# Optimization experiments

Hardware: AMD Instinct MI355X
Metric: run time of the kernel (lower is better)

Reference implementation:

```python
import jax, jax.numpy as jnp
import numpy as np

VOCAB = 40000
EMB = 128
INNER = 128
Q_LEN = 20


def setup_inputs() -> dict:
    key = jax.random.key(0)
    ks = jax.random.split(key, 16)
    B, S, NB = 32, 512, 20
    std = 0.1
    inp = {
        "memories": jax.random.normal(ks[0], (B, S, NB, EMB), jnp.float32),
        "stories": jax.random.normal(ks[1], (B, S, EMB), jnp.float32),
        "stories_mask": jnp.ones((B, S), jnp.float32),
        "queries": jax.random.randint(ks[2], (B, Q_LEN), 0, VOCAB, jnp.int32),
        "keys": jax.random.randint(ks[3], (NB,), 0, VOCAB, jnp.int32),
        # learned parameters
        "emb_table": jax.random.normal(ks[4], (VOCAB, EMB), jnp.float32) * std,
        "mult_mask": jnp.ones((Q_LEN, EMB), jnp.float32),
        "A": jax.random.normal(ks[5], (EMB, INNER), jnp.float32) * std,
        "Bm": jax.random.normal(ks[6], (EMB, INNER), jnp.float32) * std,
        "C": jax.random.normal(ks[7], (EMB, INNER), jnp.float32) * std,
        "v": jnp.ones((INNER,), jnp.float32),
        "D": jax.random.normal(ks[8], (EMB, INNER), jnp.float32) * std,
        "E": jax.random.normal(ks[9], (EMB, INNER), jnp.float32) * std,
        "F": jax.random.normal(ks[10], (EMB, INNER), jnp.float32) * std,
        "w": jnp.ones((INNER,), jnp.float32),
        "H": jax.random.normal(ks[11], (EMB, EMB), jnp.float32) * std,
        "R": jax.random.normal(ks[12], (EMB, VOCAB), jnp.float32) * std,
    }
    return inp


def reference(memories, stories, stories_mask, queries, keys,
              emb_table, mult_mask, A, Bm, C, v, D, E, F, w, H, R):
    # _reduce_query: embed tokens, apply positional multiplicative mask, sum over positions
    u = jnp.sum(emb_table[queries] * mult_mask, axis=1)            # [B, emb]

    # intratemporal (Bahdanau-style) attention over memory blocks
    ia = jnp.einsum('bsne,ei->bsni', memories, A)                  # [B,S,NB,inner]
    kb = emb_table[keys] @ Bm                                      # [NB,inner]
    qc = u @ C                                                     # [B,inner]
    intr_align = jnp.sum(v * jnp.tanh(ia + kb[None, None] + qc[:, None, None]), axis=3)  # [B,S,NB]
    intr_attn = jax.nn.softmax(intr_align, axis=2)[..., None]      # [B,S,NB,1]
    temporal_memory = jnp.sum(intr_attn * memories, axis=2)        # [B,S,emb]

    # temporal attention over story sentences (with sentence term E, softmax activation)
    td = temporal_memory @ D                                       # [B,S,inner]
    te = stories @ E                                               # [B,S,inner]
    tf = (u @ F)[:, None]                                          # [B,1,inner]
    temporal_align_unmasked = jnp.sum(w * jnp.tanh(td + te + tf), axis=2)  # [B,S]
    temporal_align = temporal_align_unmasked * stories_mask
    # softmax branch: additive -inf mask where stories_mask == 0 (inf*0 NaNs zeroed in torch)
    masked_logits = jnp.where(stories_mask != 0, temporal_align, -jnp.inf)
    temporal_attn = jax.nn.softmax(masked_logits, axis=1)          # [B,S]

    # output readout (standard memory-network head)
    o = jnp.sum(temporal_attn[..., None] * temporal_memory, axis=1)  # [B,emb]
    logits = (o + u @ H) @ R                                         # [B,vocab]
    return logits
```

## Files before the change

### kernel.cpp

```cpp
#include <hip/hip_runtime.h>
#include <hip/hip_bf16.h>

#define B_   32
#define S_   512
#define NB_  20
#define EMB_ 128
#define VOC_ 40000

typedef float f32x4 __attribute__((ext_vector_type(4)));
typedef _Float16 f16x8 __attribute__((ext_vector_type(8)));
typedef __fp16 fp16x2 __attribute__((ext_vector_type(2)));

union FragH { uint4 u; f16x8 h; };
union H2 { fp16x2 h; unsigned u; };

__device__ __forceinline__ unsigned pk2(float a, float b){
  H2 t; t.h = __builtin_amdgcn_cvt_pkrtz(a, b);
  return t.u;
}
__device__ __forceinline__ unsigned short f2h(float x){
  _Float16 h = (_Float16)x;
  return __builtin_bit_cast(unsigned short, h);
}
__device__ __forceinline__ float tanh_fast(float x){
  float xx = fminf(fmaxf(x, -15.f), 15.f);
  float e2 = __builtin_amdgcn_exp2f(xx * 2.8853900817779268f);
  float r  = __builtin_amdgcn_rcpf(e2 + 1.f);
  return fmaf(-2.f, r, 1.f);
}


__global__ __launch_bounds__(128) void prep_kernel(
    const int* __restrict__ queries, const int* __restrict__ keys,
    const float* __restrict__ emb, const float* __restrict__ mmask,
    const float* __restrict__ A, const float* __restrict__ Bm,
    const float* __restrict__ C, const float* __restrict__ D,
    const float* __restrict__ E, const float* __restrict__ F,
    const float* __restrict__ H,
    float* __restrict__ qc_w, float* __restrict__ tf_w,
    float* __restrict__ uh_w, float* __restrict__ kb_w,
    unsigned short* __restrict__ afrag, unsigned short* __restrict__ w2frag)
{
  int bid = blockIdx.x, tid = threadIdx.x;
  if (bid < 32) {
    __shared__ float ulds[128];
    int b = bid;
    float s = 0.f;
    for (int q=0;q<NB_;q++){
      int tok = queries[b*NB_+q];
      s += emb[tok*128+tid]*mmask[q*128+tid];
    }
    ulds[tid] = s;
    __syncthreads();
    float sq=0.f, sf=0.f, sh=0.f;
    for (int e=0;e<128;e++){
      float uv = ulds[e];
      sq += uv*C[e*128+tid];
      sf += uv*F[e*128+tid];
      sh += uv*H[e*128+tid];
    }
    qc_w[b*128+tid]=sq; tf_w[b*128+tid]=sf; uh_w[b*128+tid]=sh;
  } else if (bid < 52) {
    __shared__ float ek[128];
    int n = bid-32;
    int tok = keys[n];
    ek[tid] = emb[tok*128+tid];
    __syncthreads();
    float s=0.f;
    for (int e=0;e<128;e++) s += ek[e]*Bm[e*128+tid];
    kb_w[n*128+tid] = s;
  } else if (bid < 60) {
    int a = bid-52;
    for (int cc=0;cc<2;cc++){
      int c = (a*128+tid)*2+cc;
      int lane = c&63, kc = (c>>6)&3, nt = c>>8;
      int n2 = nt*16 + (lane&15);
      int k0 = kc*32 + (lane>>4)*8;
      alignas(16) unsigned short t[8];
      #pragma unroll
      for (int j=0;j<8;j++) t[j] = f2h(A[(k0+j)*128+n2]);
      *(uint4*)(afrag + c*8) = *(const uint4*)t;
    }
  } else {
    int wb = bid-60;
    for (int cc=0;cc<2;cc++){
      int c = (wb*128+tid)*2+cc;
      int lane = c&63, kc = (c>>6)&7, nt = c>>9;
      int n2 = nt*16 + (lane&15);
      int k0 = kc*32 + (lane>>4)*8;
      alignas(16) unsigned short t[8];
      #pragma unroll
      for (int j=0;j<8;j++){
        int k = k0+j;
        float x = (k<128) ? D[k*128+n2] : E[(k-128)*128+n2];
        t[j] = f2h(x);
      }
      *(uint4*)(w2frag + c*8) = *(const uint4*)t;
    }
  }
}

__global__ __launch_bounds__(256) void k2_kernel(
    const float* __restrict__ mem, const unsigned short* __restrict__ afrag,
    const float* __restrict__ kb_w, const float* __restrict__ qc_w,
    const float* __restrict__ vvec,
    const float* __restrict__ stories, const unsigned short* __restrict__ w2frag,
    const float* __restrict__ tf_w, const float* __restrict__ wvec,
    const float* __restrict__ smask,
    unsigned short* __restrict__ tm_h, float* __restrict__ talign_w)
{
  __shared__ unsigned short mfr[5*4*64*8];
  __shared__ float alignP[4*80];
  __shared__ float aligns[80];
  __shared__ float attns[80];
  __shared__ float partial2[16];

  int g = blockIdx.x, tid = threadIdx.x;
  int b = g >> 7;

  int p2 = tid>>6, e0 = (tid&63)*2;
  float2 sto = *(const float2*)(stories + ((size_t)(g*4+p2))*128 + e0);

  {
    int kq = (tid&31)*4;
    int kgs = kq>>5, s2s = (kq>>3)&3, offs = kq&7;
    int r0 = tid>>5;
    int cbs = s2s ^ ((kgs&1)<<2);
    int slot_e = (s2s<<4) | ((r0 ^ cbs) & 15);
    int slot_o = (s2s<<4) | (((r0^8) ^ cbs) & 15);
    unsigned addr_e = (unsigned)((kgs*64 + slot_e)*16 + offs*2);
    unsigned addr_o = (unsigned)((kgs*64 + slot_o)*16 + offs*2);
    const float4* gm = (const float4*)(mem) + (size_t)g*2560 + tid;
    #pragma unroll
    for (int mt=0; mt<5; ++mt){
      float4 d0 = gm[(2*mt)*256];
      float4 d1 = gm[(2*mt+1)*256];
      *(uint2*)((char*)mfr + addr_e + mt*4096) = make_uint2(pk2(d0.x,d0.y), pk2(d0.z,d0.w));
      *(uint2*)((char*)mfr + addr_o + mt*4096) = make_uint2(pk2(d1.x,d1.y), pk2(d1.z,d1.w));
    }
  }
  __syncthreads();

  int w = tid>>6, lane = tid&63;
  int lo16 = lane & 15, hi16 = lane >> 4;

  {
    f32x4 acc[5][2];
    #pragma unroll
    for (int mt=0;mt<5;mt++){ acc[mt][0]=(f32x4)(0.f); acc[mt][1]=(f32x4)(0.f); }

    #pragma unroll
    for (int kc=0;kc<4;kc++){
      FragH b0, b1;
      b0.u = *(const uint4*)(afrag + ((size_t)((2*w)*4+kc)*64 + lane)*8);
      b1.u = *(const uint4*)(afrag + ((size_t)((2*w+1)*4+kc)*64 + lane)*8);
      int slot = (hi16<<4) | ((lo16 ^ hi16 ^ ((kc&1)<<2)) & 15);
      #pragma unroll
      for (int mt=0;mt<5;mt++){
        FragH a;
        a.u = *(const uint4*)(mfr + ((mt*4+kc)*64 + slot)*8);
        acc[mt][0] = __builtin_amdgcn_mfma_f32_16x16x32_f16(a.h, b0.h, acc[mt][0], 0,0,0);
        acc[mt][1] = __builtin_amdgcn_mfma_f32_16x16x32_f16(a.h, b1.h, acc[mt][1], 0,0,0);
      }
    }

    int i0 = w*32 + lo16, i1 = i0 + 16;
    float qc0 = qc_w[b*128+i0], qc1 = qc_w[b*128+i1];
    float vv0 = vvec[i0],       vv1 = vvec[i1];
    const float* kb0 = kb_w + i0;
    #pragma unroll
    for (int mt=0;mt<5;mt++){
      #pragma unroll
      for (int r=0;r<4;r++){
        unsigned row = mt*16 + hi16*4 + r;
        unsigned p = row/20u;
        unsigned n = row - p*20u;
        float z0 = acc[mt][0][r] + kb0[n*128]    + qc0;
        float z1 = acc[mt][1][r] + kb0[n*128+16] + qc1;
        float part = vv0*tanh_fast(z0) + vv1*tanh_fast(z1);
        part += __shfl_xor(part, 1);
        part += __shfl_xor(part, 2);
        part += __shfl_xor(part, 4);
        part += __shfl_xor(part, 8);
        if (lo16 == 0) alignP[w*80+row] = part;
      }
    }
  }
  __syncthreads();
  if (tid < 80){
    aligns[tid] = alignP[tid] + alignP[80+tid] + alignP[160+tid] + alignP[240+tid];
  }
  __syncthreads();
  if (tid < 4){
    float mx = -1e30f;
    for (int n=0;n<NB_;n++) mx = fmaxf(mx, aligns[tid*NB_+n]);
    float s = 0.f;
    for (int n=0;n<NB_;n++){ float e = __expf(aligns[tid*NB_+n]-mx); attns[tid*NB_+n]=e; s+=e; }
    float inv = 1.f/s;
    for (int n=0;n<NB_;n++) attns[tid*NB_+n] *= inv;
  }
  __syncthreads();

  unsigned otm;
  {
    int kg = e0>>5, s2 = (e0>>3)&3;
    int cb = s2 ^ ((kg&1)<<2);
    unsigned base = (unsigned)((kg*64 + (s2<<4))*16 + (e0&7)*2);
    float2 o = make_float2(0.f,0.f);
    #define TM_STEP(ROW) { \
      H2 q; q.u = *(const unsigned*)((const char*)mfr + base + (((ROW)>>4)*4096) + ((((ROW)&15) ^ cb) & 15)*16); \
      float a = attns[(ROW)]; \
      o.x += a*(float)q.h[0]; \
      o.y += a*(float)q.h[1]; }
    #define TM_20(P) { \
      TM_STEP((P)*20+0)  TM_STEP((P)*20+1)  TM_STEP((P)*20+2)  TM_STEP((P)*20+3)  \
      TM_STEP((P)*20+4)  TM_STEP((P)*20+5)  TM_STEP((P)*20+6)  TM_STEP((P)*20+7)  \
      TM_STEP((P)*20+8)  TM_STEP((P)*20+9)  TM_STEP((P)*20+10) TM_STEP((P)*20+11) \
      TM_STEP((P)*20+12) TM_STEP((P)*20+13) TM_STEP((P)*20+14) TM_STEP((P)*20+15) \
      TM_STEP((P)*20+16) TM_STEP((P)*20+17) TM_STEP((P)*20+18) TM_STEP((P)*20+19) }
    switch(p2){
      case 0: TM_20(0) break;
      case 1: TM_20(1) break;
      case 2: TM_20(2) break;
      default: TM_20(3) break;
    }
    otm = pk2(o.x, o.y);
    *(unsigned*)(tm_h + ((size_t)g*4+p2)*128 + e0) = otm;
  }
  __syncthreads();

  {
    int kc = e0>>5;
    int lane2 = (((e0>>3)&3)<<4) | p2;
    *(unsigned*)(mfr + (kc*64+lane2)*8 + (e0&7)) = otm;
    *(unsigned*)(mfr + ((kc+4)*64+lane2)*8 + (e0&7)) = pk2(sto.x, sto.y);
  }
  __syncthreads();

  {
    f32x4 acc0 = (f32x4)(0.f), acc1 = (f32x4)(0.f);
    #pragma unroll
    for (int kc=0;kc<8;kc++){
      FragH af, b0, b1;
      af.u = *(const uint4*)(mfr + (kc*64+lane)*8);
      b0.u = *(const uint4*)(w2frag + ((size_t)((2*w)*8+kc)*64+lane)*8);
      b1.u = *(const uint4*)(w2frag + ((size_t)((2*w+1)*8+kc)*64+lane)*8);
      acc0 = __builtin_amdgcn_mfma_f32_16x16x32_f16(af.h, b0.h, acc0, 0,0,0);
      acc1 = __builtin_amdgcn_mfma_f32_16x16x32_f16(af.h, b1.h, acc1, 0,0,0);
    }
    if (hi16 == 0){
      #pragma unroll
      for (int r=0;r<4;r++){
        int i0 = (2*w)*16+lo16;
        float part = wvec[i0]*tanh_fast(acc0[r] + tf_w[b*128+i0]);
        int i1 = (2*w+1)*16+lo16;
        part += wvec[i1]*tanh_fast(acc1[r] + tf_w[b*128+i1]);
        part += __shfl_xor(part,1);
        part += __shfl_xor(part,2);
        part += __shfl_xor(part,4);
        part += __shfl_xor(part,8);
        if (lo16==0) partial2[w*4+r] = part;
      }
    }
  }
  __syncthreads();
  if (tid<4){
    float ta = partial2[tid]+partial2[4+tid]+partial2[8+tid]+partial2[12+tid];
    int flat = g*4+tid;
    float m = smask[flat];
    talign_w[flat] = (m != 0.0f) ? ta*m : -INFINITY;
  }
}

__global__ __launch_bounds__(256) void k3_kernel(
    const float* __restrict__ talign_w, const unsigned short* __restrict__ tm_h,
    const float* __restrict__ uh_w, float* __restrict__ ov_w)
{
  __shared__ float attn[512];
  __shared__ float red[256];
  __shared__ float2 red2[256];
  int bid = blockIdx.x, tid = threadIdx.x;
  int b = bid >> 3, ec = bid & 7;

  float v0 = talign_w[b*512+tid];
  float v1 = talign_w[b*512+256+tid];
  red[tid] = fmaxf(v0,v1);
  __syncthreads();
  for (int s=128;s>0;s>>=1){ if (tid<s) red[tid]=fmaxf(red[tid],red[tid+s]); __syncthreads(); }
  float M = red[0];
  __syncthreads();
  float e0v = __expf(v0-M), e1v = __expf(v1-M);
  red[tid] = e0v+e1v;
  __syncthreads();
  for (int s=128;s>0;s>>=1){ if (tid<s) red[tid]+=red[tid+s]; __syncthreads(); }
  float invZ = 1.f/red[0];
  attn[tid] = e0v*invZ;
  attn[256+tid] = e1v*invZ;
  __syncthreads();

  int e = ec*16 + (tid&7)*2;
  int sg = tid>>3;
  const unsigned short* tmb = tm_h + ((size_t)b*512 + sg*16)*128 + e;
  float2 a2 = make_float2(0.f,0.f);
  #pragma unroll 8
  for (int i=0;i<16;i++){
    H2 q; q.u = *(const unsigned*)(tmb + (size_t)i*128);
    float at = attn[sg*16+i];
    a2.x += at*(float)q.h[0];
    a2.y += at*(float)q.h[1];
  }
  red2[tid] = a2;
  __syncthreads();
  for (int s=128;s>=8;s>>=1){
    if (tid<s){ red2[tid].x += red2[tid+s].x; red2[tid].y += red2[tid+s].y; }
    __syncthreads();
  }
  if (tid<8){
    int e2 = ec*16 + tid*2;
    ov_w[b*128+e2]   = red2[tid].x + uh_w[b*128+e2];
    ov_w[b*128+e2+1] = red2[tid].y + uh_w[b*128+e2+1];
  }
}

__global__ __launch_bounds__(256) void k4_kernel(
    const float* __restrict__ ov_w, const float* __restrict__ R,
    float* __restrict__ out)
{
  int tid = threadIdx.x;
  int j = blockIdx.x*128 + (tid&63)*2;
  if (j >= VOC_) return;
  int bh = tid>>6;
  const float* ovb = ov_w + bh*8*128;
  float2 acc[8];
  #pragma unroll
  for (int bb=0;bb<8;bb++) acc[bb]=make_float2(0.f,0.f);
  for (int e=0;e<128;e+=4){
    float2 r0 = *(const float2*)(&R[(size_t)(e+0)*VOC_ + j]);
    float2 r1 = *(const float2*)(&R[(size_t)(e+1)*VOC_ + j]);
    float2 r2 = *(const float2*)(&R[(size_t)(e+2)*VOC_ + j]);
    float2 r3 = *(const float2*)(&R[(size_t)(e+3)*VOC_ + j]);
    #pragma unroll
    for (int bb=0;bb<8;bb++){
      float4 o = *(const float4*)(&ovb[bb*128+e]);
      acc[bb].x += o.x*r0.x + o.y*r1.x + o.z*r2.x + o.w*r3.x;
      acc[bb].y += o.x*r0.y + o.y*r1.y + o.z*r2.y + o.w*r3.y;
    }
  }
  #pragma unroll
  for (int bb=0;bb<8;bb++)
    *(float2*)(&out[(size_t)(bh*8+bb)*VOC_ + j]) = acc[bb];
}

extern "C" void kernel_launch(void* const* d_in, const int* in_sizes, int n_in,
                              void* d_out, int out_size, void* d_ws, size_t ws_size,
                              hipStream_t stream)
{
  const float* mem    = (const float*)d_in[0];
  const float* stories= (const float*)d_in[1];
  const float* smask  = (const float*)d_in[2];
  const int*   queries= (const int*)d_in[3];
  const int*   keys   = (const int*)d_in[4];
  const float* emb    = (const float*)d_in[5];
  const float* mmask  = (const float*)d_in[6];
  const float* A      = (const float*)d_in[7];
  const float* Bm     = (const float*)d_in[8];
  const float* C      = (const float*)d_in[9];
  const float* vvec   = (const float*)d_in[10];
  const float* D      = (const float*)d_in[11];
  const float* E      = (const float*)d_in[12];
  const float* F      = (const float*)d_in[13];
  const float* wvec   = (const float*)d_in[14];
  const float* H      = (const float*)d_in[15];
  const float* R      = (const float*)d_in[16];
  float* out = (float*)d_out;

  char* ws = (char*)d_ws;
  float* qc_w             = (float*)(ws + 0);
  float* tf_w             = (float*)(ws + 16384);
  float* uh_w             = (float*)(ws + 32768);
  float* kb_w             = (float*)(ws + 49152);
  unsigned short* afrag   = (unsigned short*)(ws + 60416);
  unsigned short* w2frag  = (unsigned short*)(ws + 93184);
  unsigned short* tm_h    = (unsigned short*)(ws + 158720);
  float* talign_w         = (float*)(ws + 4353024);
  float* ov_w             = (float*)(ws + 4418560);

  prep_kernel<<<76,128,0,stream>>>(queries, keys, emb, mmask, A, Bm, C, D, E, F, H,
                                   qc_w, tf_w, uh_w, kb_w, afrag, w2frag);
  k2_kernel<<<4096,256,0,stream>>>(mem, afrag, kb_w, qc_w, vvec,
                                   stories, w2frag, tf_w, wvec, smask,
                                   tm_h, talign_w);
  k3_kernel<<<256,256,0,stream>>>(talign_w, tm_h, uh_w, ov_w);
  k4_kernel<<<313,256,0,stream>>>(ov_w, R, out);
}
```

Measured before the change: 368.5 us.

## Process four tiles per block in k2 with register prefetch of next memory tile

k2 now loops over four consecutive 4-sentence tiles per block, with a quarter as many blocks. While the current tile is being computed, the next tile's memories and stories are loaded into registers and written to LDS once the current tile has finished reading it. The A-weight fragments and per-batch vectors are loaded into registers once per block instead of once per tile. The softmax is now a wave-parallel shuffle reduction rather than four serial threads, and a separate LDS buffer holds the second GEMM's operands. The aim is to hide global-memory latency and amortise setup, at the cost of higher register pressure (launch_bounds 256,4) and fewer blocks to balance across CUs.

```diff
diff --git a/kernel.cpp b/kernel.cpp
--- a/kernel.cpp
+++ b/kernel.cpp
@@ -100,7 +100,7 @@
   }
 }
 
-__global__ __launch_bounds__(256) void k2_kernel(
+__global__ __launch_bounds__(256,4) void k2_kernel(
     const float* __restrict__ mem, const unsigned short* __restrict__ afrag,
     const float* __restrict__ kb_w, const float* __restrict__ qc_w,
     const float* __restrict__ vvec,
@@ -110,64 +110,90 @@
     unsigned short* __restrict__ tm_h, float* __restrict__ talign_w)
 {
   __shared__ unsigned short mfr[5*4*64*8];
+  __shared__ unsigned short a2f[512*8];
   __shared__ float alignP[4*80];
-  __shared__ float aligns[80];
   __shared__ float attns[80];
   __shared__ float partial2[16];
 
-  int g = blockIdx.x, tid = threadIdx.x;
-  int b = g >> 7;
-
-  int p2 = tid>>6, e0 = (tid&63)*2;
-  float2 sto = *(const float2*)(stories + ((size_t)(g*4+p2))*128 + e0);
-
-  {
-    int kq = (tid&31)*4;
-    int kgs = kq>>5, s2s = (kq>>3)&3, offs = kq&7;
-    int r0 = tid>>5;
-    int cbs = s2s ^ ((kgs&1)<<2);
-    int slot_e = (s2s<<4) | ((r0 ^ cbs) & 15);
-    int slot_o = (s2s<<4) | (((r0^8) ^ cbs) & 15);
-    unsigned addr_e = (unsigned)((kgs*64 + slot_e)*16 + offs*2);
-    unsigned addr_o = (unsigned)((kgs*64 + slot_o)*16 + offs*2);
-    const float4* gm = (const float4*)(mem) + (size_t)g*2560 + tid;
-    #pragma unroll
-    for (int mt=0; mt<5; ++mt){
-      float4 d0 = gm[(2*mt)*256];
-      float4 d1 = gm[(2*mt+1)*256];
-      *(uint2*)((char*)mfr + addr_e + mt*4096) = make_uint2(pk2(d0.x,d0.y), pk2(d0.z,d0.w));
-      *(uint2*)((char*)mfr + addr_o + mt*4096) = make_uint2(pk2(d1.x,d1.y), pk2(d1.z,d1.w));
-    }
-  }
-  __syncthreads();
+  const int T = 4;
+  int tid = threadIdx.x;
+  int g0 = blockIdx.x * T;
+  int b = g0 >> 7;
 
   int w = tid>>6, lane = tid&63;
   int lo16 = lane & 15, hi16 = lane >> 4;
-
-  {
+  int p2 = tid>>6, e0 = (tid&63)*2;
+
+  int kq = (tid&31)*4;
+  int kgs = kq>>5, s2s = (kq>>3)&3, offs = kq&7;
+  int r0 = tid>>5;
+  int cbs = s2s ^ ((kgs&1)<<2);
+  unsigned addr_e = (unsigned)((kgs*64 + ((s2s<<4) | ((r0 ^ cbs) & 15)))*16 + offs*2);
+  unsigned addr_o = (unsigned)((kgs*64 + ((s2s<<4) | (((r0^8) ^ cbs) & 15)))*16 + offs*2);
+
+  int i0 = w*32 + lo16, i1 = i0 + 16;
+  float qc0 = qc_w[b*128+i0], qc1 = qc_w[b*128+i1];
+  float vv0 = vvec[i0],       vv1 = vvec[i1];
+  float tf0 = tf_w[b*128+i0], tf1 = tf_w[b*128+i1];
+  float wv0 = wvec[i0],       wv1 = wvec[i1];
+  const float* kb0 = kb_w + i0;
+
+  FragH bf0[4], bf1[4];
+  #pragma unroll
+  for (int kc=0;kc<4;kc++){
+    bf0[kc].u = *(const uint4*)(afrag + ((size_t)((2*w)*4+kc)*64 + lane)*8);
+    bf1[kc].u = *(const uint4*)(afrag + ((size_t)((2*w+1)*4+kc)*64 + lane)*8);
+  }
+
+  float4 pf[10];
+  float2 sto, sto_n;
+
+  auto load_tile = [&](int g){
+    const float4* gmt = (const float4*)(mem) + (size_t)g*2560 + tid;
+    #pragma unroll
+    for (int mt=0;mt<5;mt++){
+      pf[2*mt]   = gmt[(2*mt)*256];
+      pf[2*mt+1] = gmt[(2*mt+1)*256];
+    }
+  };
+  auto store_tile = [&](){
+    #pragma unroll
+    for (int mt=0;mt<5;mt++){
+      *(uint2*)((char*)mfr + addr_e + mt*4096) =
+          make_uint2(pk2(pf[2*mt].x,pf[2*mt].y), pk2(pf[2*mt].z,pf[2*mt].w));
+      *(uint2*)((char*)mfr + addr_o + mt*4096) =
+          make_uint2(pk2(pf[2*mt+1].x,pf[2*mt+1].y), pk2(pf[2*mt+1].z,pf[2*mt+1].w));
+    }
+  };
+
+  load_tile(g0);
+  sto = *(const float2*)(stories + ((size_t)(g0*4+p2))*128 + e0);
+  store_tile();
+  __syncthreads();
+
+  for (int t=0; t<T; ++t){
+    int g = g0 + t;
+
     f32x4 acc[5][2];
     #pragma unroll
     for (int mt=0;mt<5;mt++){ acc[mt][0]=(f32x4)(0.f); acc[mt][1]=(f32x4)(0.f); }
-
     #pragma unroll
     for (int kc=0;kc<4;kc++){
-      FragH b0, b1;
-      b0.u = *(const uint4*)(afrag + ((size_t)((2*w)*4+kc)*64 + lane)*8);
-      b1.u = *(const uint4*)(afrag + ((size_t)((2*w+1)*4+kc)*64 + lane)*8);
       int slot = (hi16<<4) | ((lo16 ^ hi16 ^ ((kc&1)<<2)) & 15);
       #pragma unroll
       for (int mt=0;mt<5;mt++){
         FragH a;
         a.u = *(const uint4*)(mfr + ((mt*4+kc)*64 + slot)*8);
-        acc[mt][0] = __builtin_amdgcn_mfma_f32_16x16x32_f16(a.h, b0.h, acc[mt][0], 0,0,0);
-        acc[mt][1] = __builtin_amdgcn_mfma_f32_16x16x32_f16(a.h, b1.h, acc[mt][1], 0,0,0);
-      }
-    }
-
-    int i0 = w*32 + lo16, i1 = i0 + 16;
-    float qc0 = qc_w[b*128+i0], qc1 = qc_w[b*128+i1];
-    float vv0 = vvec[i0],       vv1 = vvec[i1];
-    const float* kb0 = kb_w + i0;
+        acc[mt][0] = __builtin_amdgcn_mfma_f32_16x16x32_f16(a.h, bf0[kc].h, acc[mt][0], 0,0,0);
+        acc[mt][1] = __builtin_amdgcn_mfma_f32_16x16x32_f16(a.h, bf1[kc].h, acc[mt][1], 0,0,0);
+      }
+    }
+    if (t > 0 && tid < 4){
+      float ta = partial2[tid]+partial2[4+tid]+partial2[8+tid]+partial2[12+tid];
+      int flat = (g-1)*4+tid;
+      float m = smask[flat];
+      talign_w[flat] = (m != 0.0f) ? ta*m : -INFINITY;
+    }
     #pragma unroll
     for (int mt=0;mt<5;mt++){
       #pragma unroll
@@ -185,88 +211,94 @@
         if (lo16 == 0) alignP[w*80+row] = part;
       }
     }
-  }
-  __syncthreads();
-  if (tid < 80){
-    aligns[tid] = alignP[tid] + alignP[80+tid] + alignP[160+tid] + alignP[240+tid];
-  }
-  __syncthreads();
+    __syncthreads();
+
+    if (t+1 < T){
+      load_tile(g+1);
+      sto_n = *(const float2*)(stories + ((size_t)((g+1)*4+p2))*128 + e0);
+    }
+    {
+      float av = -1e30f;
+      if (lane < 20){
+        int idx = w*20 + lane;
+        av = alignP[idx] + alignP[80+idx] + alignP[160+idx] + alignP[240+idx];
+      }
+      float mx = av;
+      #pragma unroll
+      for (int d=1; d<32; d<<=1) mx = fmaxf(mx, __shfl_xor(mx, d));
+      mx = fmaxf(mx, __shfl_xor(mx, 32));
+      float ev = (lane<20) ? __expf(av - mx) : 0.f;
+      float sm = ev;
+      #pragma unroll
+      for (int d=1; d<64; d<<=1) sm += __shfl_xor(sm, d);
+      if (lane<20) attns[w*20+lane] = ev * __builtin_amdgcn_rcpf(sm);
+    }
+    __syncthreads();
+
+    unsigned otm;
+    {
+      int kg = e0>>5, s2 = (e0>>3)&3;
+      int cb = s2 ^ ((kg&1)<<2);
+      unsigned base = (unsigned)((kg*64 + (s2<<4))*16 + (e0&7)*2);
+      float2 o = make_float2(0.f,0.f);
+      #define TM_STEP(ROW) { \
+        H2 q; q.u = *(const unsigned*)((const char*)mfr + base + (((ROW)>>4)*4096) + ((((ROW)&15) ^ cb) & 15)*16); \
+        float a = attns[(ROW)]; \
+        o.x += a*(float)q.h[0]; \
+        o.y += a*(float)q.h[1]; }
+      #define TM_20(P) { \
+        TM_STEP((P)*20+0)  TM_STEP((P)*20+1)  TM_STEP((P)*20+2)  TM_STEP((P)*20+3)  \
+        TM_STEP((P)*20+4)  TM_STEP((P)*20+5)  TM_STEP((P)*20+6)  TM_STEP((P)*20+7)  \
+        TM_STEP((P)*20+8)  TM_STEP((P)*20+9)  TM_STEP((P)*20+10) TM_STEP((P)*20+11) \
+        TM_STEP((P)*20+12) TM_STEP((P)*20+13) TM_STEP((P)*20+14) TM_STEP((P)*20+15) \
+        TM_STEP((P)*20+16) TM_STEP((P)*20+17) TM_STEP((P)*20+18) TM_STEP((P)*20+19) }
+      switch(p2){
+        case 0: TM_20(0) break;
+        case 1: TM_20(1) break;
+        case 2: TM_20(2) break;
+        default: TM_20(3) break;
+      }
+      otm = pk2(o.x, o.y);
+      *(unsigned*)(tm_h + ((size_t)g*4+p2)*128 + e0) = otm;
+      int kcA = e0>>5;
+      int lane2 = (((e0>>3)&3)<<4) | p2;
+      *(unsigned*)(a2f + (kcA*64+lane2)*8 + (e0&7)) = otm;
+      *(unsigned*)(a2f + ((kcA+4)*64+lane2)*8 + (e0&7)) = pk2(sto.x, sto.y);
+    }
+    __syncthreads();
+
+    if (t+1 < T){
+      store_tile();
+      sto = sto_n;
+    }
+    {
+      f32x4 acc0 = (f32x4)(0.f), acc1 = (f32x4)(0.f);
+      #pragma unroll
+      for (int kc=0;kc<8;kc++){
+        FragH af, b0, b1;
+        af.u = *(const uint4*)(a2f + (kc*64+lane)*8);
+        b0.u = *(const uint4*)(w2frag + ((size_t)((2*w)*8+kc)*64+lane)*8);
+        b1.u = *(const uint4*)(w2frag + ((size_t)((2*w+1)*8+kc)*64+lane)*8);
+        acc0 = __builtin_amdgcn_mfma_f32_16x16x32_f16(af.h, b0.h, acc0, 0,0,0);
+        acc1 = __builtin_amdgcn_mfma_f32_16x16x32_f16(af.h, b1.h, acc1, 0,0,0);
+      }
+      if (hi16 == 0){
+        #pragma unroll
+        for (int r=0;r<4;r++){
+          float part = wv0*tanh_fast(acc0[r] + tf0) + wv1*tanh_fast(acc1[r] + tf1);
+          part += __shfl_xor(part,1);
+          part += __shfl_xor(part,2);
+          part += __shfl_xor(part,4);
+          part += __shfl_xor(part,8);
+          if (lo16==0) partial2[w*4+r] = part;
+        }
+      }
+    }
+    __syncthreads();
+  }
   if (tid < 4){
-    float mx = -1e30f;
-    for (int n=0;n<NB_;n++) mx = fmaxf(mx, aligns[tid*NB_+n]);
-    float s = 0.f;
-    for (int n=0;n<NB_;n++){ float e = __expf(aligns[tid*NB_+n]-mx); attns[tid*NB_+n]=e; s+=e; }
-    float inv = 1.f/s;
-    for (int n=0;n<NB_;n++) attns[tid*NB_+n] *= inv;
-  }
-  __syncthreads();
-
-  unsigned otm;
-  {
-    int kg = e0>>5, s2 = (e0>>3)&3;
-    int cb = s2 ^ ((kg&1)<<2);
-    unsigned base = (unsigned)((kg*64 + (s2<<4))*16 + (e0&7)*2);
-    float2 o = make_float2(0.f,0.f);
-    #define TM_STEP(ROW) { \
-      H2 q; q.u = *(const unsigned*)((const char*)mfr + base + (((ROW)>>4)*4096) + ((((ROW)&15) ^ cb) & 15)*16); \
-      float a = attns[(ROW)]; \
-      o.x += a*(float)q.h[0]; \
-      o.y += a*(float)q.h[1]; }
-    #define TM_20(P) { \
-      TM_STEP((P)*20+0)  TM_STEP((P)*20+1)  TM_STEP((P)*20+2)  TM_STEP((P)*20+3)  \
-      TM_STEP((P)*20+4)  TM_STEP((P)*20+5)  TM_STEP((P)*20+6)  TM_STEP((P)*20+7)  \
-      TM_STEP((P)*20+8)  TM_STEP((P)*20+9)  TM_STEP((P)*20+10) TM_STEP((P)*20+11) \
-      TM_STEP((P)*20+12) TM_STEP((P)*20+13) TM_STEP((P)*20+14) TM_STEP((P)*20+15) \
-      TM_STEP((P)*20+16) TM_STEP((P)*20+17) TM_STEP((P)*20+18) TM_STEP((P)*20+19) }
-    switch(p2){
-      case 0: TM_20(0) break;
-      case 1: TM_20(1) break;
-      case 2: TM_20(2) break;
-      default: TM_20(3) break;
-    }
-    otm = pk2(o.x, o.y);
-    *(unsigned*)(tm_h + ((size_t)g*4+p2)*128 + e0) = otm;
-  }
-  __syncthreads();
-
-  {
-    int kc = e0>>5;
-    int lane2 = (((e0>>3)&3)<<4) | p2;
-    *(unsigned*)(mfr + (kc*64+lane2)*8 + (e0&7)) = otm;
-    *(unsigned*)(mfr + ((kc+4)*64+lane2)*8 + (e0&7)) = pk2(sto.x, sto.y);
-  }
-  __syncthreads();
-
-  {
-    f32x4 acc0 = (f32x4)(0.f), acc1 = (f32x4)(0.f);
-    #pragma unroll
-    for (int kc=0;kc<8;kc++){
-      FragH af, b0, b1;
-      af.u = *(const uint4*)(mfr + (kc*64+lane)*8);
-      b0.u = *(const uint4*)(w2frag + ((size_t)((2*w)*8+kc)*64+lane)*8);
-      b1.u = *(const uint4*)(w2frag + ((size_t)((2*w+1)*8+kc)*64+lane)*8);
-      acc0 = __builtin_amdgcn_mfma_f32_16x16x32_f16(af.h, b0.h, acc0, 0,0,0);
-      acc1 = __builtin_amdgcn_mfma_f32_16x16x32_f16(af.h, b1.h, acc1, 0,0,0);
-    }
-    if (hi16 == 0){
-      #pragma unroll
-      for (int r=0;r<4;r++){
-        int i0 = (2*w)*16+lo16;
-        float part = wvec[i0]*tanh_fast(acc0[r] + tf_w[b*128+i0]);
-        int i1 = (2*w+1)*16+lo16;
-        part += wvec[i1]*tanh_fast(acc1[r] + tf_w[b*128+i1]);
-        part += __shfl_xor(part,1);
-        part += __shfl_xor(part,2);
-        part += __shfl_xor(part,4);
-        part += __shfl_xor(part,8);
-        if (lo16==0) partial2[w*4+r] = part;
-      }
-    }
-  }
-  __syncthreads();
-  if (tid<4){
     float ta = partial2[tid]+partial2[4+tid]+partial2[8+tid]+partial2[12+tid];
-    int flat = g*4+tid;
+    int flat = (g0+T-1)*4+tid;
     float m = smask[flat];
     talign_w[flat] = (m != 0.0f) ? ta*m : -INFINITY;
   }
@@ -387,7 +419,7 @@
 
   prep_kernel<<<76,128,0,stream>>>(queries, keys, emb, mmask, A, Bm, C, D, E, F, H,
                                    qc_w, tf_w, uh_w, kb_w, afrag, w2frag);
-  k2_kernel<<<4096,256,0,stream>>>(mem, afrag, kb_w, qc_w, vvec,
+  k2_kernel<<<1024,256,0,stream>>>(mem, afrag, kb_w, qc_w, vvec,
                                    stories, w2frag, tf_w, wvec, smask,
                                    tm_h, talign_w);
   k3_kernel<<<256,256,0,stream>>>(talign_w, tm_h, uh_w, ov_w);
```

Measured after the change: 503.4 us. 36.6% more time.

## Precombine key and query bias per batch, warp-level softmax, trim tanh clamp

Applied to the files above, without the earlier changes.

The prep kernel now builds a combined per-batch, per-block bias table (kb + qc) across 640 extra blocks, so the main kernel adds one value instead of two and drops the division that mapped a row to its block index. The three-step block softmax (shared-memory reduction plus four serial threads) becomes a per-wave shuffle reduction, which removes a __syncthreads barrier. Loop-invariant vector loads are hoisted, and the clamp inside tanh_fast is removed; without it, large arguments rely on exp2 overflowing to infinity and the reciprocal then giving zero. The cost is a larger prep launch and a bigger bias table to read in the main kernel.

```diff
diff --git a/kernel.cpp b/kernel.cpp
--- a/kernel.cpp
+++ b/kernel.cpp
@@ -23,8 +23,7 @@
   return __builtin_bit_cast(unsigned short, h);
 }
 __device__ __forceinline__ float tanh_fast(float x){
-  float xx = fminf(fmaxf(x, -15.f), 15.f);
-  float e2 = __builtin_amdgcn_exp2f(xx * 2.8853900817779268f);
+  float e2 = __builtin_amdgcn_exp2f(x * 2.8853900817779268f);
   float r  = __builtin_amdgcn_rcpf(e2 + 1.f);
   return fmaf(-2.f, r, 1.f);
 }
@@ -37,8 +36,8 @@
     const float* __restrict__ C, const float* __restrict__ D,
     const float* __restrict__ E, const float* __restrict__ F,
     const float* __restrict__ H,
-    float* __restrict__ qc_w, float* __restrict__ tf_w,
-    float* __restrict__ uh_w, float* __restrict__ kb_w,
+    float* __restrict__ tf_w, float* __restrict__ uh_w,
+    float* __restrict__ kbq_w,
     unsigned short* __restrict__ afrag, unsigned short* __restrict__ w2frag)
 {
   int bid = blockIdx.x, tid = threadIdx.x;
@@ -52,25 +51,33 @@
     }
     ulds[tid] = s;
     __syncthreads();
-    float sq=0.f, sf=0.f, sh=0.f;
+    float sf=0.f, sh=0.f;
     for (int e=0;e<128;e++){
       float uv = ulds[e];
-      sq += uv*C[e*128+tid];
       sf += uv*F[e*128+tid];
       sh += uv*H[e*128+tid];
     }
-    qc_w[b*128+tid]=sq; tf_w[b*128+tid]=sf; uh_w[b*128+tid]=sh;
-  } else if (bid < 52) {
+    tf_w[b*128+tid]=sf; uh_w[b*128+tid]=sh;
+  } else if (bid < 672) {
+    __shared__ float ulds[128];
     __shared__ float ek[128];
-    int n = bid-32;
-    int tok = keys[n];
-    ek[tid] = emb[tok*128+tid];
+    int idx = bid-32;
+    int b = idx/20, n = idx - b*20;
+    float s = 0.f;
+    for (int q=0;q<NB_;q++){
+      int tok = queries[b*NB_+q];
+      s += emb[tok*128+tid]*mmask[q*128+tid];
+    }
+    ulds[tid] = s;
+    ek[tid] = emb[keys[n]*128+tid];
     __syncthreads();
-    float s=0.f;
-    for (int e=0;e<128;e++) s += ek[e]*Bm[e*128+tid];
-    kb_w[n*128+tid] = s;
-  } else if (bid < 60) {
-    int a = bid-52;
+    float acc = 0.f;
+    for (int e=0;e<128;e++){
+      acc += ulds[e]*C[e*128+tid] + ek[e]*Bm[e*128+tid];
+    }
+    kbq_w[idx*128+tid] = acc;
+  } else if (bid < 680) {
+    int a = bid-672;
     for (int cc=0;cc<2;cc++){
       int c = (a*128+tid)*2+cc;
       int lane = c&63, kc = (c>>6)&3, nt = c>>8;
@@ -82,7 +89,7 @@
       *(uint4*)(afrag + c*8) = *(const uint4*)t;
     }
   } else {
-    int wb = bid-60;
+    int wb = bid-680;
     for (int cc=0;cc<2;cc++){
       int c = (wb*128+tid)*2+cc;
       int lane = c&63, kc = (c>>6)&7, nt = c>>9;
@@ -102,8 +109,7 @@
 
 __global__ __launch_bounds__(256) void k2_kernel(
     const float* __restrict__ mem, const unsigned short* __restrict__ afrag,
-    const float* __restrict__ kb_w, const float* __restrict__ qc_w,
-    const float* __restrict__ vvec,
+    const float* __restrict__ kbq_w, const float* __restrict__ vvec,
     const float* __restrict__ stories, const unsigned short* __restrict__ w2frag,
     const float* __restrict__ tf_w, const float* __restrict__ wvec,
     const float* __restrict__ smask,
@@ -111,14 +117,16 @@
 {
   __shared__ unsigned short mfr[5*4*64*8];
   __shared__ float alignP[4*80];
-  __shared__ float aligns[80];
   __shared__ float attns[80];
   __shared__ float partial2[16];
 
   int g = blockIdx.x, tid = threadIdx.x;
   int b = g >> 7;
 
-  int p2 = tid>>6, e0 = (tid&63)*2;
+  int w = tid>>6, lane = tid&63;
+  int lo16 = lane & 15, hi16 = lane >> 4;
+  int p2 = w, e0 = (tid&63)*2;
+
   float2 sto = *(const float2*)(stories + ((size_t)(g*4+p2))*128 + e0);
 
   {
@@ -141,65 +149,71 @@
   }
   __syncthreads();
 
-  int w = tid>>6, lane = tid&63;
-  int lo16 = lane & 15, hi16 = lane >> 4;
+  int i0 = w*32 + lo16, i1 = i0 + 16;
+  float vv0 = vvec[i0],       vv1 = vvec[i1];
+  float tf0 = tf_w[b*128+i0], tf1 = tf_w[b*128+i1];
+  float wv0 = wvec[i0],       wv1 = wvec[i1];
+  const float* kbq0 = kbq_w + b*(NB_*128) + i0;
+
+  f32x4 acc[5][2];
+  #pragma unroll
+  for (int mt=0;mt<5;mt++){ acc[mt][0]=(f32x4)(0.f); acc[mt][1]=(f32x4)(0.f); }
+  #pragma unroll
+  for (int kc=0;kc<4;kc++){
+    FragH b0, b1;
+    b0.u = *(const uint4*)(afrag + ((size_t)((2*w)*4+kc)*64 + lane)*8);
+    b1.u = *(const uint4*)(afrag + ((size_t)((2*w+1)*4+kc)*64 + lane)*8);
+    int slot = (hi16<<4) | ((lo16 ^ hi16 ^ ((kc&1)<<2)) & 15);
+    #pragma unroll
+    for (int mt=0;mt<5;mt++){
+      FragH a;
+      a.u = *(const uint4*)(mfr + ((mt*4+kc)*64 + slot)*8);
+      acc[mt][0] = __builtin_amdgcn_mfma_f32_16x16x32_f16(a.h, b0.h, acc[mt][0], 0,0,0);
+      acc[mt][1] = __builtin_amdgcn_mfma_f32_16x16x32_f16(a.h, b1.h, acc[mt][1], 0,0,0);
+    }
+  }
+
+  #define EPI_BODY(HH) { \
+    _Pragma("unroll") \
+    for (int mt=0;mt<5;mt++){ \
+      _Pragma("unroll") \
+      for (int r=0;r<4;r++){ \
+        const int row = mt*16 + (HH) + r; \
+        const int n = row % 20; \
+        float z0 = acc[mt][0][r] + kbq0[n*128]; \
+        float z1 = acc[mt][1][r] + kbq0[n*128+16]; \
+        float part = vv0*tanh_fast(z0) + vv1*tanh_fast(z1); \
+        part += __shfl_xor(part, 1); \
+        part += __shfl_xor(part, 2); \
+        part += __shfl_xor(part, 4); \
+        part += __shfl_xor(part, 8); \
+        if (lo16 == 0) alignP[w*80+row] = part; \
+      } \
+    } }
+  switch(hi16){
+    case 0:  EPI_BODY(0)  break;
+    case 1:  EPI_BODY(4)  break;
+    case 2:  EPI_BODY(8)  break;
+    default: EPI_BODY(12) break;
+  }
+  #undef EPI_BODY
+  __syncthreads();
 
   {
-    f32x4 acc[5][2];
-    #pragma unroll
-    for (int mt=0;mt<5;mt++){ acc[mt][0]=(f32x4)(0.f); acc[mt][1]=(f32x4)(0.f); }
-
-    #pragma unroll
-    for (int kc=0;kc<4;kc++){
-      FragH b0, b1;
-      b0.u = *(const uint4*)(afrag + ((size_t)((2*w)*4+kc)*64 + lane)*8);
-      b1.u = *(const uint4*)(afrag + ((size_t)((2*w+1)*4+kc)*64 + lane)*8);
-      int slot = (hi16<<4) | ((lo16 ^ hi16 ^ ((kc&1)<<2)) & 15);
-      #pragma unroll
-      for (int mt=0;mt<5;mt++){
-        FragH a;
-        a.u = *(const uint4*)(mfr + ((mt*4+kc)*64 + slot)*8);
-        acc[mt][0] = __builtin_amdgcn_mfma_f32_16x16x32_f16(a.h, b0.h, acc[mt][0], 0,0,0);
-        acc[mt][1] = __builtin_amdgcn_mfma_f32_16x16x32_f16(a.h, b1.h, acc[mt][1], 0,0,0);
-      }
-    }
-
-    int i0 = w*32 + lo16, i1 = i0 + 16;
-    float qc0 = qc_w[b*128+i0], qc1 = qc_w[b*128+i1];
-    float vv0 = vvec[i0],       vv1 = vvec[i1];
-    const float* kb0 = kb_w + i0;
-    #pragma unroll
-    for (int mt=0;mt<5;mt++){
-      #pragma unroll
-      for (int r=0;r<4;r++){
-        unsigned row = mt*16 + hi16*4 + r;
-        unsigned p = row/20u;
-        unsigned n = row - p*20u;
-        float z0 = acc[mt][0][r] + kb0[n*128]    + qc0;
-        float z1 = acc[mt][1][r] + kb0[n*128+16] + qc1;
-        float part = vv0*tanh_fast(z0) + vv1*tanh_fast(z1);
-        part += __shfl_xor(part, 1);
-        part += __shfl_xor(part, 2);
-        part += __shfl_xor(part, 4);
-        part += __shfl_xor(part, 8);
-        if (lo16 == 0) alignP[w*80+row] = part;
-      }
-    }
-  }
-  __syncthreads();
-  if (tid < 80){
-    aligns[tid] = alignP[tid] + alignP[80+tid] + alignP[160+tid] + alignP[240+tid];
-  }
-  __syncthreads();
-  if (tid < 4){
-    float mx = -1e30f;
-    for (int n=0;n<NB_;n++) mx = fmaxf(mx, aligns[tid*NB_+n]);
-    float s = 0.f;
-    for (int n=0;n<NB_;n++){ float e = __expf(aligns[tid*NB_+n]-mx); attns[tid*NB_+n]=e; s+=e; }
-    float inv = 1.f/s;
-    for (int n=0;n<NB_;n++) attns[tid*NB_+n] *= inv;
-  }
-  __syncthreads();
+    float av = -1e30f;
+    if (lane < 20){
+      int idx = w*20 + lane;
+      av = alignP[idx] + alignP[80+idx] + alignP[160+idx] + alignP[240+idx];
+    }
+    float mx = av;
+    #pragma unroll
+    for (int d=1; d<64; d<<=1) mx = fmaxf(mx, __shfl_xor(mx, d));
+    float ev = (lane<20) ? __expf(av - mx) : 0.f;
+    float sm = ev;
+    #pragma unroll
+    for (int d=1; d<64; d<<=1) sm += __shfl_xor(sm, d);
+    if (lane<20) attns[w*20+lane] = ev * __builtin_amdgcn_rcpf(sm);
+  }
 
   unsigned otm;
   {
@@ -224,16 +238,18 @@
       case 2: TM_20(2) break;
       default: TM_20(3) break;
     }
+    #undef TM_20
+    #undef TM_STEP
     otm = pk2(o.x, o.y);
     *(unsigned*)(tm_h + ((size_t)g*4+p2)*128 + e0) = otm;
   }
   __syncthreads();
 
   {
-    int kc = e0>>5;
+    int kcA = e0>>5;
     int lane2 = (((e0>>3)&3)<<4) | p2;
-    *(unsigned*)(mfr + (kc*64+lane2)*8 + (e0&7)) = otm;
-    *(unsigned*)(mfr + ((kc+4)*64+lane2)*8 + (e0&7)) = pk2(sto.x, sto.y);
+    *(unsigned*)(mfr + (kcA*64+lane2)*8 + (e0&7)) = otm;
+    *(unsigned*)(mfr + ((kcA+4)*64+lane2)*8 + (e0&7)) = pk2(sto.x, sto.y);
   }
   __syncthreads();
 
@@ -251,10 +267,7 @@
     if (hi16 == 0){
       #pragma unroll
       for (int r=0;r<4;r++){
-        int i0 = (2*w)*16+lo16;
-        float part = wvec[i0]*tanh_fast(acc0[r] + tf_w[b*128+i0]);
-        int i1 = (2*w+1)*16+lo16;
-        part += wvec[i1]*tanh_fast(acc1[r] + tf_w[b*128+i1]);
+        float part = wv0*tanh_fast(acc0[r] + tf0) + wv1*tanh_fast(acc1[r] + tf1);
         part += __shfl_xor(part,1);
         part += __shfl_xor(part,2);
         part += __shfl_xor(part,4);
@@ -264,7 +277,8 @@
     }
   }
   __syncthreads();
-  if (tid<4){
+
+  if (tid < 4){
     float ta = partial2[tid]+partial2[4+tid]+partial2[8+tid]+partial2[12+tid];
     int flat = g*4+tid;
     float m = smask[flat];
@@ -375,19 +389,18 @@
   float* out = (float*)d_out;
 
   char* ws = (char*)d_ws;
-  float* qc_w             = (float*)(ws + 0);
-  float* tf_w             = (float*)(ws + 16384);
-  float* uh_w             = (float*)(ws + 32768);
-  float* kb_w             = (float*)(ws + 49152);
-  unsigned short* afrag   = (unsigned short*)(ws + 60416);
-  unsigned short* w2frag  = (unsigned short*)(ws + 93184);
-  unsigned short* tm_h    = (unsigned short*)(ws + 158720);
-  float* talign_w         = (float*)(ws + 4353024);
-  float* ov_w             = (float*)(ws + 4418560);
-
-  prep_kernel<<<76,128,0,stream>>>(queries, keys, emb, mmask, A, Bm, C, D, E, F, H,
-                                   qc_w, tf_w, uh_w, kb_w, afrag, w2frag);
-  k2_kernel<<<4096,256,0,stream>>>(mem, afrag, kb_w, qc_w, vvec,
+  float* tf_w             = (float*)(ws + 0);
+  float* uh_w             = (float*)(ws + 16384);
+  float* kbq_w            = (float*)(ws + 32768);
+  unsigned short* afrag   = (unsigned short*)(ws + 360448);
+  unsigned short* w2frag  = (unsigned short*)(ws + 393216);
+  unsigned short* tm_h    = (unsigned short*)(ws + 458752);
+  float* talign_w         = (float*)(ws + 4653056);
+  float* ov_w             = (float*)(ws + 4718592);
+
+  prep_kernel<<<696,128,0,stream>>>(queries, keys, emb, mmask, A, Bm, C, D, E, F, H,
+                                    tf_w, uh_w, kbq_w, afrag, w2frag);
+  k2_kernel<<<4096,256,0,stream>>>(mem, afrag, kbq_w, vvec,
                                    stories, w2frag, tf_w, wvec, smask,
                                    tm_h, talign_w);
   k3_kernel<<<256,256,0,stream>>>(talign_w, tm_h, uh_w, ov_w);
```

Result: slower. 436.4 us (+18.4%).
